# Performance work log

Hardware: AMD Instinct MI355X
Metric: run time of the kernel (lower is better)

The kernel has to match this reference:

```python
import jax, jax.numpy as jnp
import numpy as np

T, D, I, E, TOPK = 4096, 1024, 1024, 8, 2

def setup_inputs() -> dict:
    key = jax.random.key(0)
    ks = jax.random.split(key, 5)
    scale = 1.0 / np.sqrt(D)
    return {
        "x": jax.random.normal(ks[0], (T, D), dtype=jnp.float32),
        "gate_w": jax.random.normal(ks[1], (E, D), dtype=jnp.float32) * scale,
        "w1": jax.random.normal(ks[2], (E, I, D), dtype=jnp.float32) * scale,
        "w3": jax.random.normal(ks[3], (E, I, D), dtype=jnp.float32) * scale,
        "w2": jax.random.normal(ks[4], (E, D, I), dtype=jnp.float32) * (1.0 / np.sqrt(I)),
    }

def reference(x, gate_w, w1, w3, w2):
    # Gate: softmax over experts, then top-k (weights are pre-top-k softmax probs)
    scores = jax.nn.softmax(x @ gate_w.T, axis=-1)          # [T, E]
    weights, indices = jax.lax.top_k(scores, TOPK)          # [T, K], [T, K]

    # Dense SwiGLU for every expert over all tokens (faithful to masked loop:
    # experts are bias-free so expert(x*mask) == mask * expert(x))
    h = jnp.einsum('td,eid->eti', x, w1)                    # [E, T, I]
    g = jnp.einsum('td,eid->eti', x, w3)                    # [E, T, I]
    a = jax.nn.silu(h) * g                                  # [E, T, I]
    out = jnp.einsum('eti,edi->etd', a, w2)                 # [E, T, D]

    # Gather each token's top-k expert outputs and combine with routing weights
    out_t = jnp.transpose(out, (1, 0, 2))                   # [T, E, D]
    sel = jnp.take_along_axis(out_t, indices[:, :, None], axis=1)  # [T, K, D]
    y = jnp.sum(sel * weights[:, :, None], axis=1)          # [T, D]
    return y
```

## Files before the change

kernel.cpp:

```cpp
#include <hip/hip_runtime.h>
#include <hip/hip_bf16.h>

typedef unsigned short u16;
typedef unsigned int u32;
typedef __attribute__((ext_vector_type(8))) short bf16x8;
typedef __attribute__((ext_vector_type(4))) float f32x4;

#define NEXP 8
#define NTOK 4096
#define DDIM 1024
#define MAX_TILES 80

__device__ __forceinline__ u16 f2bf(float f) {
    u32 u = __float_as_uint(f);
    u += 0x7fff + ((u >> 16) & 1);
    return (u16)(u >> 16);
}

__device__ __forceinline__ void gload16(const void* g, void* l) {
    __builtin_amdgcn_global_load_lds((const __attribute__((address_space(1))) u32*)g,
                                     (__attribute__((address_space(3))) u32*)l, 16, 0, 0);
}

__global__ __launch_bounds__(256) void cvt_w_kernel(const float* __restrict__ w1,
                                                    const float* __restrict__ w3,
                                                    const float* __restrict__ w2,
                                                    u16* __restrict__ out) {
    const int N8 = 3145728;
    int stride = gridDim.x * blockDim.x;
    for (int i = blockIdx.x * blockDim.x + threadIdx.x; i < N8; i += stride) {
        const float* src;
        if (i < 1048576)       src = w1 + (size_t)i * 8;
        else if (i < 2097152)  src = w3 + ((size_t)i - 1048576) * 8;
        else                   src = w2 + ((size_t)i - 2097152) * 8;
        float4 a = ((const float4*)src)[0], b = ((const float4*)src)[1];
        uint4 o;
        o.x = (u32)f2bf(a.x) | ((u32)f2bf(a.y) << 16);
        o.y = (u32)f2bf(a.z) | ((u32)f2bf(a.w) << 16);
        o.z = (u32)f2bf(b.x) | ((u32)f2bf(b.y) << 16);
        o.w = (u32)f2bf(b.z) | ((u32)f2bf(b.w) << 16);
        *(uint4*)(out + (size_t)i * 8) = o;
    }
}

__global__ __launch_bounds__(256) void gate_kernel(const float* __restrict__ x,
                                                   const float* __restrict__ gw,
                                                   int* __restrict__ t2i, float* __restrict__ t2w,
                                                   u16* __restrict__ xb) {
    int tid = threadIdx.x;
    int wv = tid >> 6, lane = tid & 63;
    int t = blockIdx.x * 4 + wv;
    const float4* xr = (const float4*)(x + (size_t)t * DDIM);
    float4 xv[4];
#pragma unroll
    for (int q = 0; q < 4; q++) xv[q] = xr[lane * 4 + q];

    uint4 o0, o1;
    o0.x = (u32)f2bf(xv[0].x) | ((u32)f2bf(xv[0].y) << 16);
    o0.y = (u32)f2bf(xv[0].z) | ((u32)f2bf(xv[0].w) << 16);
    o0.z = (u32)f2bf(xv[1].x) | ((u32)f2bf(xv[1].y) << 16);
    o0.w = (u32)f2bf(xv[1].z) | ((u32)f2bf(xv[1].w) << 16);
    o1.x = (u32)f2bf(xv[2].x) | ((u32)f2bf(xv[2].y) << 16);
    o1.y = (u32)f2bf(xv[2].z) | ((u32)f2bf(xv[2].w) << 16);
    o1.z = (u32)f2bf(xv[3].x) | ((u32)f2bf(xv[3].y) << 16);
    o1.w = (u32)f2bf(xv[3].z) | ((u32)f2bf(xv[3].w) << 16);
    uint4* xbo = (uint4*)(xb + (size_t)t * DDIM + lane * 16);
    xbo[0] = o0;
    xbo[1] = o1;

    float acc[NEXP];
#pragma unroll
    for (int e = 0; e < NEXP; e++) acc[e] = 0.f;
#pragma unroll
    for (int e = 0; e < NEXP; e++) {
#pragma unroll
        for (int q = 0; q < 4; q++) {
            float4 g = ((const float4*)gw)[e * 256 + lane * 4 + q];
            acc[e] += xv[q].x * g.x + xv[q].y * g.y + xv[q].z * g.z + xv[q].w * g.w;
        }
    }
#pragma unroll
    for (int e = 0; e < NEXP; e++) {
        float v = acc[e];
#pragma unroll
        for (int off = 32; off; off >>= 1) v += __shfl_xor(v, off, 64);
        acc[e] = v;
    }
    if (lane == 0) {
        float m = acc[0];
#pragma unroll
        for (int e = 1; e < NEXP; e++) m = fmaxf(m, acc[e]);
        float p[NEXP]; float s = 0.f;
#pragma unroll
        for (int e = 0; e < NEXP; e++) { p[e] = __expf(acc[e] - m); s += p[e]; }
        float inv = 1.f / s;
        float best = -1.f, sec = -1.f; int bi = 0, si = 0;
#pragma unroll
        for (int e = 0; e < NEXP; e++) {
            float pe = p[e] * inv;
            if (pe > best) { sec = best; si = bi; best = pe; bi = e; }
            else if (pe > sec) { sec = pe; si = e; }
        }
        t2i[2 * t] = bi;  t2i[2 * t + 1] = si;
        t2w[2 * t] = best; t2w[2 * t + 1] = sec;
    }
}

__global__ __launch_bounds__(1024) void sort_kernel(const int* __restrict__ t2i,
                                                    const float* __restrict__ t2w,
                                                    int* __restrict__ ctl,
                                                    int* __restrict__ slot_token,
                                                    float* __restrict__ slot_wt) {
    __shared__ int sb[NEXP][1024];
    __shared__ int wsum[16];
    __shared__ int sex[16];
    __shared__ int stot[NEXP];
    __shared__ int soffs[NEXP + 1];
    int tid = threadIdx.x;
    int lane = tid & 63, wv = tid >> 6;

    int4 a = *(const int4*)(t2i + tid * 8);
    int4 b = *(const int4*)(t2i + tid * 8 + 4);
    int ev0 = a.x, ev1 = a.y, ev2 = a.z, ev3 = a.w;
    int ev4 = b.x, ev5 = b.y, ev6 = b.z, ev7 = b.w;
    u32 cnt = (1u << (ev0 * 4)) + (1u << (ev1 * 4)) + (1u << (ev2 * 4)) + (1u << (ev3 * 4)) +
              (1u << (ev4 * 4)) + (1u << (ev5 * 4)) + (1u << (ev6 * 4)) + (1u << (ev7 * 4));

    for (int e = 0; e < NEXP; e++) {
        int v = (cnt >> (e * 4)) & 15;
        int inc = v;
#pragma unroll
        for (int off = 1; off < 64; off <<= 1) {
            int n = __shfl_up(inc, off, 64);
            if (lane >= off) inc += n;
        }
        if (lane == 63) wsum[wv] = inc;
        __syncthreads();
        if (wv == 0) {
            int w = (lane < 16) ? wsum[lane] : 0;
            int winc = w;
#pragma unroll
            for (int off = 1; off < 16; off <<= 1) {
                int n = __shfl_up(winc, off, 64);
                if (lane >= off) winc += n;
            }
            if (lane < 16) sex[lane] = winc - w;
            if (lane == 15) stot[e] = winc;
        }
        __syncthreads();
        sb[e][tid] = sex[wv] + inc - v;
        __syncthreads();
    }
    if (tid == 0) {
        int o = 0, tt = 0;
        for (int e = 0; e < NEXP; e++) {
            soffs[e] = o;
            ctl[16 + e] = o;
            ctl[280 + e] = tt;
            int n = stot[e];
            for (int r = 0; r < n; r += 128) {
                ctl[32 + tt] = e; ctl[112 + tt] = o + r; ctl[192 + tt] = o + n; tt++;
            }
            o += n;
        }
        soffs[NEXP] = o; ctl[24] = o; ctl[25] = tt; ctl[288] = tt;
    }
    __syncthreads();
#pragma unroll
    for (int j = 0; j < 8; j++) {
        int e;
        switch (j) {
            case 0: e = ev0; break; case 1: e = ev1; break; case 2: e = ev2; break;
            case 3: e = ev3; break; case 4: e = ev4; break; case 5: e = ev5; break;
            case 6: e = ev6; break; default: e = ev7; break;
        }
        int base = sb[e][tid];
        sb[e][tid] = base + 1;
        int slot = soffs[e] + base;
        int p = tid * 8 + j;
        slot_token[slot] = p >> 1;
        slot_wt[slot] = t2w[p];
    }
}

template <int MODE>
__global__ __launch_bounds__(256, 4) void moe_gemm_kernel(
    const u16* __restrict__ Amat, const u16* __restrict__ B1g, const u16* __restrict__ B2g,
    u16* __restrict__ OutB, float* __restrict__ OutY,
    const int* __restrict__ ctl, const int* __restrict__ slot_token,
    const float* __restrict__ slot_wt) {
    constexpr int BN = (MODE == 0) ? 64 : 128;
    constexpr int NB = BN / 32;
    constexpr int NCB = DDIM / BN;
    constexpr int NK = 32;

    int ntiles = ctl[25];
    int N = ntiles * NCB;
    int bid = blockIdx.x;
    if (bid >= N) return;
    int q = N >> 3, r = N & 7;
    int xcd = bid & 7, seq = bid >> 3;
    int n = (xcd < r ? xcd * (q + 1) : r * (q + 1) + (xcd - r) * q) + seq;
    int e = 0, tstart = 0, tiles_e = 0, m = n;
    for (; e < NEXP; e++) {
        tstart = ctl[280 + e];
        tiles_e = ctl[281 + e] - tstart;
        int sz = tiles_e * NCB;
        if (m < sz) break;
        m -= sz;
    }
    if (e == NEXP) return;
    int cb = m / tiles_e;
    int tt = tstart + (m - cb * tiles_e);
    int rowbase = ctl[112 + tt];
    int segend = ctl[192 + tt];

    __shared__ __align__(16) u16 smem[2 * 128 * 32 + 2 * BN * 32 + ((MODE == 0) ? 2 * 64 * 32 : 0)];
    u16* sA = smem;
    u16* sB1 = smem + 2 * 128 * 32;
    u16* sB2 = sB1 + 2 * BN * 32;

    int tid = threadIdx.x;
    int lane = tid & 63;
    int wv = tid >> 6;
    int wrow = wv >> 1, wcol = wv & 1;
    int lr = lane >> 2;
    int cS = (((lane & 3) ^ ((lane >> 3) & 3)) << 3);
    int l15 = lane & 15, hi = lane >> 4;
    int csr = ((hi ^ ((l15 >> 1) & 3)) << 3);

    u32 rowA[2];
#pragma unroll
    for (int i = 0; i < 2; i++) {
        int slot = rowbase + wv * 32 + i * 16 + lr;
        if (slot >= segend) slot = rowbase;
        int src = (MODE == 0) ? slot_token[slot] : slot;
        rowA[i] = (u32)src * 1024;
    }
    u32 rowB[2];
    if constexpr (MODE == 0) {
        int rr = cb * 64 + wv * 16 + lr;
        rowB[0] = (u32)e * 1048576 + (u32)rr * 1024;
        rowB[1] = 0;
    } else {
#pragma unroll
        for (int i = 0; i < 2; i++) {
            int rr = cb * 128 + wv * 32 + i * 16 + lr;
            rowB[i] = (u32)e * 1048576 + (u32)rr * 1024;
        }
    }

    f32x4 accH[4][NB], accG[(MODE == 0) ? 4 : 1][(MODE == 0) ? NB : 1];
    f32x4 zero = {0.f, 0.f, 0.f, 0.f};
#pragma unroll
    for (int m2 = 0; m2 < 4; m2++)
#pragma unroll
        for (int nn = 0; nn < NB; nn++) accH[m2][nn] = zero;
    if constexpr (MODE == 0) {
#pragma unroll
        for (int m2 = 0; m2 < 4; m2++)
#pragma unroll
            for (int nn = 0; nn < NB; nn++) accG[m2][nn] = zero;
    }

    auto stage = [&](int buf, int kt) {
        int k0 = kt * 32 + cS;
        gload16(Amat + rowA[0] + k0, sA + buf * 4096 + (wv * 32) * 32);
        gload16(Amat + rowA[1] + k0, sA + buf * 4096 + (wv * 32 + 16) * 32);
        if constexpr (MODE == 0) {
            gload16(B1g + rowB[0] + k0, sB1 + buf * 2048 + (wv * 16) * 32);
            gload16(B2g + rowB[0] + k0, sB2 + buf * 2048 + (wv * 16) * 32);
        } else {
            gload16(B1g + rowB[0] + k0, sB1 + buf * 4096 + (wv * 32) * 32);
            gload16(B1g + rowB[1] + k0, sB1 + buf * 4096 + (wv * 32 + 16) * 32);
        }
    };

    auto compute = [&](int buf) {
        bf16x8 av[4];
#pragma unroll
        for (int m2 = 0; m2 < 4; m2++) {
            int rr = wrow * 64 + m2 * 16 + l15;
            av[m2] = *(const bf16x8*)(sA + buf * 4096 + rr * 32 + csr);
        }
        bf16x8 b1v[NB];
#pragma unroll
        for (int nn = 0; nn < NB; nn++) {
            int rr = wcol * (BN / 2) + nn * 16 + l15;
            b1v[nn] = *(const bf16x8*)(sB1 + buf * (BN * 32) + rr * 32 + csr);
        }
        if constexpr (MODE == 0) {
            bf16x8 b2v[NB];
#pragma unroll
            for (int nn = 0; nn < NB; nn++) {
                int rr = wcol * (BN / 2) + nn * 16 + l15;
                b2v[nn] = *(const bf16x8*)(sB2 + buf * (BN * 32) + rr * 32 + csr);
            }
#pragma unroll
            for (int m2 = 0; m2 < 4; m2++)
#pragma unroll
                for (int nn = 0; nn < NB; nn++) {
                    accH[m2][nn] = __builtin_amdgcn_mfma_f32_16x16x32_bf16(av[m2], b1v[nn], accH[m2][nn], 0, 0, 0);
                    accG[m2][nn] = __builtin_amdgcn_mfma_f32_16x16x32_bf16(av[m2], b2v[nn], accG[m2][nn], 0, 0, 0);
                }
        } else {
#pragma unroll
            for (int m2 = 0; m2 < 4; m2++)
#pragma unroll
                for (int nn = 0; nn < NB; nn++)
                    accH[m2][nn] = __builtin_amdgcn_mfma_f32_16x16x32_bf16(av[m2], b1v[nn], accH[m2][nn], 0, 0, 0);
        }
    };

    stage(0, 0);
    for (int kt = 0; kt < NK; ++kt) {
        __syncthreads();
        if (kt + 1 < NK) stage((kt + 1) & 1, kt + 1);
        compute(kt & 1);
    }

    int colblock = cb * BN + wcol * (BN / 2);
#pragma unroll
    for (int m2 = 0; m2 < 4; m2++) {
        int slotbase = rowbase + wrow * 64 + m2 * 16 + hi * 4;
#pragma unroll
        for (int nn = 0; nn < NB; nn++) {
            int col = colblock + nn * 16 + l15;
#pragma unroll
            for (int j = 0; j < 4; j++) {
                int slot = slotbase + j;
                if (slot < segend) {
                    if constexpr (MODE == 0) {
                        float h = accH[m2][nn][j], g = accG[m2][nn][j];
                        float aa = (h / (1.f + __expf(-h))) * g;
                        OutB[(size_t)slot * 1024 + col] = f2bf(aa);
                    } else {
                        int tok = slot_token[slot];
                        float wgt = slot_wt[slot];
                        unsafeAtomicAdd(&OutY[(size_t)tok * 1024 + col], accH[m2][nn][j] * wgt);
                    }
                }
            }
        }
    }
}

extern "C" void kernel_launch(void* const* d_in, const int* in_sizes, int n_in,
                              void* d_out, int out_size, void* d_ws, size_t ws_size,
                              hipStream_t stream) {
    const float* x  = (const float*)d_in[0];
    const float* gw = (const float*)d_in[1];
    const float* w1 = (const float*)d_in[2];
    const float* w3 = (const float*)d_in[3];
    const float* w2 = (const float*)d_in[4];
    float* y = (float*)d_out;
    char* ws = (char*)d_ws;

    int*   ctl        = (int*)ws;
    int*   t2i        = (int*)(ws + 4096);
    float* t2w        = (float*)(ws + 4096 + 32768);
    int*   slot_token = (int*)(ws + 4096 + 65536);
    float* slot_wt    = (float*)(ws + 4096 + 98304);
    u16*   xb   = (u16*)(ws + 262144);
    u16*   w1b  = xb  + (size_t)4194304;
    u16*   w3b  = w1b + (size_t)8388608;
    u16*   w2b  = w3b + (size_t)8388608;
    u16*   Abuf = w2b + (size_t)8388608;

    hipMemsetAsync(ctl, 0, 4096, stream);
    hipMemsetAsync(y, 0, (size_t)out_size * sizeof(float), stream);

    cvt_w_kernel<<<2048, 256, 0, stream>>>(w1, w3, w2, w1b);
    gate_kernel<<<1024, 256, 0, stream>>>(x, gw, t2i, t2w, xb);
    sort_kernel<<<1, 1024, 0, stream>>>(t2i, t2w, ctl, slot_token, slot_wt);

    moe_gemm_kernel<0><<<MAX_TILES * 16, 256, 0, stream>>>(
        xb, w1b, w3b, Abuf, nullptr, ctl, slot_token, slot_wt);
    moe_gemm_kernel<1><<<MAX_TILES * 8, 256, 0, stream>>>(
        Abuf, w2b, nullptr, nullptr, y, ctl, slot_token, slot_wt);
}
```

Measured before the change: 164.0 us.

## Fuse gate and weight conversion kernels, shrink down-proj tile, raise occupancy

Merges the weight fp32-to-bf16 conversion into the gate kernel as extra blocks, so both run in one launch and can overlap. The down-projection GEMM now uses 64-wide column tiles instead of 128, which doubles its grid and improves SM fill for the small per-expert tile count. Launch bounds are raised to 5 and 6 waves per SIMD to push occupancy. Smaller tiles reload the A rows more often and add more atomic adds, and the tighter launch bounds may force register spills.

Result: slower. 174.2 us (+6.3%).

```diff
diff --git a/kernel.cpp b/kernel.cpp
--- a/kernel.cpp
+++ b/kernel.cpp
@@ -22,34 +22,35 @@
                                      (__attribute__((address_space(3))) u32*)l, 16, 0, 0);
 }
 
-__global__ __launch_bounds__(256) void cvt_w_kernel(const float* __restrict__ w1,
-                                                    const float* __restrict__ w3,
-                                                    const float* __restrict__ w2,
-                                                    u16* __restrict__ out) {
-    const int N8 = 3145728;
-    int stride = gridDim.x * blockDim.x;
-    for (int i = blockIdx.x * blockDim.x + threadIdx.x; i < N8; i += stride) {
-        const float* src;
-        if (i < 1048576)       src = w1 + (size_t)i * 8;
-        else if (i < 2097152)  src = w3 + ((size_t)i - 1048576) * 8;
-        else                   src = w2 + ((size_t)i - 2097152) * 8;
-        float4 a = ((const float4*)src)[0], b = ((const float4*)src)[1];
-        uint4 o;
-        o.x = (u32)f2bf(a.x) | ((u32)f2bf(a.y) << 16);
-        o.y = (u32)f2bf(a.z) | ((u32)f2bf(a.w) << 16);
-        o.z = (u32)f2bf(b.x) | ((u32)f2bf(b.y) << 16);
-        o.w = (u32)f2bf(b.z) | ((u32)f2bf(b.w) << 16);
-        *(uint4*)(out + (size_t)i * 8) = o;
-    }
-}
-
-__global__ __launch_bounds__(256) void gate_kernel(const float* __restrict__ x,
-                                                   const float* __restrict__ gw,
-                                                   int* __restrict__ t2i, float* __restrict__ t2w,
-                                                   u16* __restrict__ xb) {
+__global__ __launch_bounds__(256) void gate_cvt_kernel(const float* __restrict__ x,
+                                                       const float* __restrict__ gw,
+                                                       const float* __restrict__ w1,
+                                                       const float* __restrict__ w3,
+                                                       const float* __restrict__ w2,
+                                                       int* __restrict__ t2i, float* __restrict__ t2w,
+                                                       u16* __restrict__ xb, u16* __restrict__ wb) {
+    int bid = blockIdx.x;
     int tid = threadIdx.x;
+    if (bid >= 1024) {
+        const int N8 = 3145728;
+        int stride = 1536 * 256;
+        for (int i = (bid - 1024) * 256 + tid; i < N8; i += stride) {
+            const float* src;
+            if (i < 1048576)       src = w1 + (size_t)i * 8;
+            else if (i < 2097152)  src = w3 + ((size_t)i - 1048576) * 8;
+            else                   src = w2 + ((size_t)i - 2097152) * 8;
+            float4 a = ((const float4*)src)[0], b = ((const float4*)src)[1];
+            uint4 o;
+            o.x = (u32)f2bf(a.x) | ((u32)f2bf(a.y) << 16);
+            o.y = (u32)f2bf(a.z) | ((u32)f2bf(a.w) << 16);
+            o.z = (u32)f2bf(b.x) | ((u32)f2bf(b.y) << 16);
+            o.w = (u32)f2bf(b.z) | ((u32)f2bf(b.w) << 16);
+            *(uint4*)(wb + (size_t)i * 8) = o;
+        }
+        return;
+    }
     int wv = tid >> 6, lane = tid & 63;
-    int t = blockIdx.x * 4 + wv;
+    int t = bid * 4 + wv;
     const float4* xr = (const float4*)(x + (size_t)t * DDIM);
     float4 xv[4];
 #pragma unroll
@@ -184,14 +185,14 @@
 }
 
 template <int MODE>
-__global__ __launch_bounds__(256, 4) void moe_gemm_kernel(
+__global__ __launch_bounds__(256, (MODE == 0) ? 5 : 6) void moe_gemm_kernel(
     const u16* __restrict__ Amat, const u16* __restrict__ B1g, const u16* __restrict__ B2g,
     u16* __restrict__ OutB, float* __restrict__ OutY,
     const int* __restrict__ ctl, const int* __restrict__ slot_token,
     const float* __restrict__ slot_wt) {
-    constexpr int BN = (MODE == 0) ? 64 : 128;
-    constexpr int NB = BN / 32;
-    constexpr int NCB = DDIM / BN;
+    constexpr int BN = 64;
+    constexpr int NB = 2;
+    constexpr int NCB = 16;
     constexpr int NK = 32;
 
     int ntiles = ctl[25];
@@ -215,10 +216,10 @@
     int rowbase = ctl[112 + tt];
     int segend = ctl[192 + tt];
 
-    __shared__ __align__(16) u16 smem[2 * 128 * 32 + 2 * BN * 32 + ((MODE == 0) ? 2 * 64 * 32 : 0)];
+    __shared__ __align__(16) u16 smem[2 * 128 * 32 + 2 * 64 * 32 + ((MODE == 0) ? 2 * 64 * 32 : 0)];
     u16* sA = smem;
     u16* sB1 = smem + 2 * 128 * 32;
-    u16* sB2 = sB1 + 2 * BN * 32;
+    u16* sB2 = sB1 + 2 * 64 * 32;
 
     int tid = threadIdx.x;
     int lane = tid & 63;
@@ -237,17 +238,10 @@
         int src = (MODE == 0) ? slot_token[slot] : slot;
         rowA[i] = (u32)src * 1024;
     }
-    u32 rowB[2];
-    if constexpr (MODE == 0) {
+    u32 rowB0;
+    {
         int rr = cb * 64 + wv * 16 + lr;
-        rowB[0] = (u32)e * 1048576 + (u32)rr * 1024;
-        rowB[1] = 0;
-    } else {
-#pragma unroll
-        for (int i = 0; i < 2; i++) {
-            int rr = cb * 128 + wv * 32 + i * 16 + lr;
-            rowB[i] = (u32)e * 1048576 + (u32)rr * 1024;
-        }
+        rowB0 = (u32)e * 1048576 + (u32)rr * 1024;
     }
 
     f32x4 accH[4][NB], accG[(MODE == 0) ? 4 : 1][(MODE == 0) ? NB : 1];
@@ -267,12 +261,9 @@
         int k0 = kt * 32 + cS;
         gload16(Amat + rowA[0] + k0, sA + buf * 4096 + (wv * 32) * 32);
         gload16(Amat + rowA[1] + k0, sA + buf * 4096 + (wv * 32 + 16) * 32);
+        gload16(B1g + rowB0 + k0, sB1 + buf * 2048 + (wv * 16) * 32);
         if constexpr (MODE == 0) {
-            gload16(B1g + rowB[0] + k0, sB1 + buf * 2048 + (wv * 16) * 32);
-            gload16(B2g + rowB[0] + k0, sB2 + buf * 2048 + (wv * 16) * 32);
-        } else {
-            gload16(B1g + rowB[0] + k0, sB1 + buf * 4096 + (wv * 32) * 32);
-            gload16(B1g + rowB[1] + k0, sB1 + buf * 4096 + (wv * 32 + 16) * 32);
+            gload16(B2g + rowB0 + k0, sB2 + buf * 2048 + (wv * 16) * 32);
         }
     };
 
@@ -286,15 +277,15 @@
         bf16x8 b1v[NB];
 #pragma unroll
         for (int nn = 0; nn < NB; nn++) {
-            int rr = wcol * (BN / 2) + nn * 16 + l15;
-            b1v[nn] = *(const bf16x8*)(sB1 + buf * (BN * 32) + rr * 32 + csr);
+            int rr = wcol * 32 + nn * 16 + l15;
+            b1v[nn] = *(const bf16x8*)(sB1 + buf * 2048 + rr * 32 + csr);
         }
         if constexpr (MODE == 0) {
             bf16x8 b2v[NB];
 #pragma unroll
             for (int nn = 0; nn < NB; nn++) {
-                int rr = wcol * (BN / 2) + nn * 16 + l15;
-                b2v[nn] = *(const bf16x8*)(sB2 + buf * (BN * 32) + rr * 32 + csr);
+                int rr = wcol * 32 + nn * 16 + l15;
+                b2v[nn] = *(const bf16x8*)(sB2 + buf * 2048 + rr * 32 + csr);
             }
 #pragma unroll
             for (int m2 = 0; m2 < 4; m2++)
@@ -319,7 +310,7 @@
         compute(kt & 1);
     }
 
-    int colblock = cb * BN + wcol * (BN / 2);
+    int colblock = cb * 64 + wcol * 32;
 #pragma unroll
     for (int m2 = 0; m2 < 4; m2++) {
         int slotbase = rowbase + wrow * 64 + m2 * 16 + hi * 4;
@@ -370,12 +361,11 @@
     hipMemsetAsync(ctl, 0, 4096, stream);
     hipMemsetAsync(y, 0, (size_t)out_size * sizeof(float), stream);
 
-    cvt_w_kernel<<<2048, 256, 0, stream>>>(w1, w3, w2, w1b);
-    gate_kernel<<<1024, 256, 0, stream>>>(x, gw, t2i, t2w, xb);
+    gate_cvt_kernel<<<2560, 256, 0, stream>>>(x, gw, w1, w3, w2, t2i, t2w, xb, w1b);
     sort_kernel<<<1, 1024, 0, stream>>>(t2i, t2w, ctl, slot_token, slot_wt);
 
     moe_gemm_kernel<0><<<MAX_TILES * 16, 256, 0, stream>>>(
         xb, w1b, w3b, Abuf, nullptr, ctl, slot_token, slot_wt);
-    moe_gemm_kernel<1><<<MAX_TILES * 8, 256, 0, stream>>>(
+    moe_gemm_kernel<1><<<MAX_TILES * 16, 256, 0, stream>>>(
         Abuf, w2b, nullptr, nullptr, y, ctl, slot_token, slot_wt);
 }
```
